# Performance work log

Hardware: AMD Instinct MI355X
Metric: run time of the kernel (lower is better)

## Reference

```python
import jax, jax.numpy as jnp
import numpy as np

B, S, D, H, DFF = 2, 2048, 1024, 16, 4096
DK = D // H
EPS = float(np.finfo(np.float32).eps)  # torch RMSNorm default eps = finfo eps


def rmsnorm(x, g):
    var = jnp.mean(x * x, axis=-1, keepdims=True)
    return x * jax.lax.rsqrt(var + EPS) * g


def rope_cos_sin(seq_len, dim, base=10000.0):
    inv_freq = 1.0 / (base ** (jnp.arange(0, dim, 2, dtype=jnp.float32) / dim))
    t = jnp.arange(seq_len, dtype=jnp.float32)
    freqs = jnp.outer(t, inv_freq)            # [S, dim/2]
    emb = jnp.concatenate([freqs, freqs], -1)  # [S, dim]
    return jnp.cos(emb), jnp.sin(emb)


def rotate_half(x):
    x1, x2 = x[..., : x.shape[-1] // 2], x[..., x.shape[-1] // 2:]
    return jnp.concatenate([-x2, x1], axis=-1)


def setup_inputs() -> dict:
    key = jax.random.key(0)
    ks = jax.random.split(key, 16)
    sc = 0.02
    return {
        "x": jax.random.normal(ks[0], (B, S, D), jnp.float32),
        "wq": jax.random.normal(ks[1], (D, D), jnp.float32) * sc,
        "bq": jnp.zeros((D,), jnp.float32),
        "wk": jax.random.normal(ks[2], (D, D), jnp.float32) * sc,
        "bk": jnp.zeros((D,), jnp.float32),
        "wv": jax.random.normal(ks[3], (D, D), jnp.float32) * sc,
        "bv": jnp.zeros((D,), jnp.float32),
        "wo": jax.random.normal(ks[4], (D, D), jnp.float32) * sc,
        "bo": jnp.zeros((D,), jnp.float32),
        "w1": jax.random.normal(ks[5], (D, DFF), jnp.float32) * sc,
        "b1": jnp.zeros((DFF,), jnp.float32),
        "w2": jax.random.normal(ks[6], (DFF, D), jnp.float32) * sc,
        "b2": jnp.zeros((D,), jnp.float32),
        "g1": jnp.ones((D,), jnp.float32),
        "g2": jnp.ones((D,), jnp.float32),
    }


def reference(x, wq, bq, wk, bk, wv, bv, wo, bo, w1, b1, w2, b2, g1, g2):
    b, s, d = x.shape
    # --- self-attention sublayer (pre-RMSNorm residual) ---
    h = rmsnorm(x, g1)
    q = (h @ wq + bq).reshape(b, s, H, DK).transpose(0, 2, 1, 3)  # [B,H,S,dk]
    k = (h @ wk + bk).reshape(b, s, H, DK).transpose(0, 2, 1, 3)
    v = (h @ wv + bv).reshape(b, s, H, DK).transpose(0, 2, 1, 3)
    cos, sin = rope_cos_sin(s, DK)
    cos = cos[None, None]  # [1,1,S,dk]
    sin = sin[None, None]
    q = q * cos + rotate_half(q) * sin
    k = k * cos + rotate_half(k) * sin
    scores = jnp.einsum("bhqd,bhkd->bhqk", q, k) / jnp.sqrt(jnp.float32(DK))
    p = jax.nn.softmax(scores, axis=-1)
    o = jnp.einsum("bhqk,bhkd->bhqd", p, v)
    o = o.transpose(0, 2, 1, 3).reshape(b, s, d)
    attn_out = o @ wo + bo
    x = x + attn_out
    # --- feed-forward sublayer ---
    h2 = rmsnorm(x, g2)
    ff = jax.nn.relu(h2 @ w1 + b1) @ w2 + b2
    return x + ff
```

## Files before the change

### kernel.cpp

```cpp
#include <hip/hip_runtime.h>
#include <math.h>

typedef unsigned short u16;
typedef __attribute__((ext_vector_type(8))) short bf16x8;
typedef __attribute__((ext_vector_type(4))) float f32x4;
typedef __attribute__((ext_vector_type(4))) unsigned int u32x4;

#define B_ 2
#define S_ 2048
#define D_ 1024
#define H_ 16
#define DK_ 64
#define DFF_ 4096
#define EPS_ 1.1920928955078125e-07f
#define EXP2SC 0.18033688011112042f

__device__ __forceinline__ float bf2f(u16 u) {
  unsigned int v = ((unsigned int)u) << 16;
  return __builtin_bit_cast(float, v);
}
__device__ __forceinline__ u16 f2bf(float f) {
  unsigned int x = __builtin_bit_cast(unsigned int, f);
  x += 0x7fffu + ((x >> 16) & 1u);
  return (u16)(x >> 16);
}

#if __has_builtin(__builtin_amdgcn_exp2f)
__device__ __forceinline__ float exp2r(float x) { return __builtin_amdgcn_exp2f(x); }
#else
__device__ __forceinline__ float exp2r(float x) { return exp2f(x); }
#endif

typedef __attribute__((address_space(3))) unsigned int lds_uint;
typedef const __attribute__((address_space(1))) unsigned int glb_uint;
__device__ __forceinline__ void gload16(const void* g, void* l) {
  __builtin_amdgcn_global_load_lds((glb_uint*)g, (lds_uint*)l, 16, 0, 0);
}

template <int N>
__device__ __forceinline__ void waitcnt_vm() {
  if constexpr (N == 8) asm volatile("s_waitcnt vmcnt(8)" ::: "memory");
  else if constexpr (N == 6) asm volatile("s_waitcnt vmcnt(6)" ::: "memory");
  else if constexpr (N == 4) asm volatile("s_waitcnt vmcnt(4)" ::: "memory");
  else if constexpr (N == 3) asm volatile("s_waitcnt vmcnt(3)" ::: "memory");
  else asm volatile("s_waitcnt vmcnt(0)" ::: "memory");
}

__device__ __forceinline__ unsigned int cvtpk(float lo, float hi) {
  unsigned int d;
  asm("v_cvt_pk_bf16_f32 %0, %1, %2" : "=v"(d) : "v"(lo), "v"(hi));
  return d;
}
__device__ __forceinline__ void plswap32(unsigned int& a, unsigned int& b) {
  asm("v_permlane32_swap_b32 %0, %1" : "+v"(a), "+v"(b));
}
__device__ __forceinline__ void plswap16(unsigned int& a, unsigned int& b) {
  asm("v_permlane16_swap_b32 %0, %1" : "+v"(a), "+v"(b));
}

__device__ __forceinline__ void xcd_swizzle(int& bx, int& by) {
  const int nx = gridDim.x;
  const int nwg = nx * gridDim.y;
  const int lin = blockIdx.y * nx + blockIdx.x;
  const int swz = (lin & 7) * (nwg >> 3) + (lin >> 3);
  bx = swz % nx;
  by = swz / nx;
}

__device__ __forceinline__ void xcd_swizzle3(int& bx, int& by, int& bz) {
  const int gx = gridDim.x, gy = gridDim.y, gz = gridDim.z;
  const int nb = gx * gy * gz;
  const int lin = ((int)blockIdx.z * gy + blockIdx.y) * gx + blockIdx.x;
  const int w = (lin & 7) * (nb >> 3) + (lin >> 3);
  bz = w % gz;
  const int r = w / gz;
  bx = r % gx;
  by = r / gx;
}

__global__ __launch_bounds__(256) void prep_qkvo(
    const float* __restrict__ wq, const float* __restrict__ wk,
    const float* __restrict__ wv, const float* __restrict__ wo,
    u16* __restrict__ qkvT, u16* __restrict__ woT,
    float* __restrict__ cosT, float* __restrict__ sinT) {
  __shared__ float t[32][33];
  const int bid = blockIdx.x;
  const int tid = threadIdx.x;
  if (bid < 4096) {
    const int m = bid >> 10;
    const int tb = bid & 1023;
    const float* src = (m == 0) ? wq : (m == 1) ? wk : (m == 2) ? wv : wo;
    u16* dst = (m == 3) ? woT : qkvT + (size_t)m * D_ * D_;
    const int c0 = (tb & 31) * 32, r0 = (tb >> 5) * 32;
    const int tx = tid & 31, ty = tid >> 5;
#pragma unroll
    for (int i = 0; i < 32; i += 8)
      t[ty + i][tx] = src[(size_t)(r0 + ty + i) * D_ + (c0 + tx)];
    __syncthreads();
#pragma unroll
    for (int i = 0; i < 32; i += 8)
      dst[(size_t)(c0 + ty + i) * D_ + (r0 + tx)] = f2bf(t[tx][ty + i]);
  } else {
    const int idx = (bid - 4096) * 256 + tid;
    const int s = idx >> 5, i = idx & 31;
    double inv = exp(((double)(-2 * i) / (double)DK_) * log(10000.0));
    double ang = (double)s * inv;
    cosT[idx] = (float)cos(ang);
    sinT[idx] = (float)sin(ang);
  }
}

__global__ __launch_bounds__(256) void prep_w12(
    const float* __restrict__ w1, const float* __restrict__ w2,
    u16* __restrict__ w1T, u16* __restrict__ w2T) {
  __shared__ float t[32][33];
  const int bid = blockIdx.x;
  const int tid = threadIdx.x;
  const int tx = tid & 31, ty = tid >> 5;
  if (bid < 4096) {
    const int c0 = (bid & 127) * 32, r0 = (bid >> 7) * 32;
#pragma unroll
    for (int i = 0; i < 32; i += 8)
      t[ty + i][tx] = w1[(size_t)(r0 + ty + i) * DFF_ + (c0 + tx)];
    __syncthreads();
#pragma unroll
    for (int i = 0; i < 32; i += 8)
      w1T[(size_t)(c0 + ty + i) * D_ + (r0 + tx)] = f2bf(t[tx][ty + i]);
  } else {
    const int b2 = bid - 4096;
    const int c0 = (b2 & 31) * 32, r0 = (b2 >> 5) * 32;
#pragma unroll
    for (int i = 0; i < 32; i += 8)
      t[ty + i][tx] = w2[(size_t)(r0 + ty + i) * D_ + (c0 + tx)];
    __syncthreads();
#pragma unroll
    for (int i = 0; i < 32; i += 8)
      w2T[(size_t)(c0 + ty + i) * DFF_ + (r0 + tx)] = f2bf(t[tx][ty + i]);
  }
}

__global__ __launch_bounds__(256) void rmsnorm_k(const float* __restrict__ X,
                                                 const float* __restrict__ g,
                                                 u16* __restrict__ out) {
  const int row = blockIdx.x;
  const float* xr = X + (size_t)row * D_;
  u16* orow = out + (size_t)row * D_;
  const int tid = threadIdx.x;
  float vals[4];
  float s = 0.f;
#pragma unroll
  for (int j = 0; j < 4; j++) {
    float v = xr[tid + j * 256];
    vals[j] = v;
    s += v * v;
  }
#pragma unroll
  for (int off = 32; off > 0; off >>= 1) s += __shfl_down(s, off, 64);
  __shared__ float red[4];
  __shared__ float ssc;
  int lane = tid & 63, wave = tid >> 6;
  if (lane == 0) red[wave] = s;
  __syncthreads();
  if (tid == 0) ssc = 1.0f / sqrtf((red[0] + red[1] + red[2] + red[3]) * (1.0f / D_) + EPS_);
  __syncthreads();
  float sc = ssc;
#pragma unroll
  for (int j = 0; j < 4; j++) {
    int i = tid + j * 256;
    orow[i] = f2bf(vals[j] * sc * g[i]);
  }
}

#define GK_STAGE(BU, K0)                                                               \
  _Pragma("unroll")                                                                    \
  for (int c = wave; c < BM / 16; c += 4) {                                            \
    const u16* gp = gkA + (size_t)(m0 + c * 16 + lrow) * gkLD + (K0) + lcol;           \
    gload16(gp, (char*)As + __builtin_amdgcn_readfirstlane((BU) * (BM * 64) + c * 1024)); \
  }                                                                                    \
  _Pragma("unroll")                                                                    \
  for (int c = wave; c < BN / 16; c += 4) {                                            \
    const u16* gp = gkB + (size_t)(n0 + c * 16 + lrow) * gkLD + (K0) + lcol;           \
    gload16(gp, (char*)Bs + __builtin_amdgcn_readfirstlane((BU) * (BN * 64) + c * 1024)); \
  }

#define GK_COMPUTE(BU)                                                                 \
  {                                                                                    \
    bf16x8 af[WR], bfv[WC];                                                            \
    _Pragma("unroll")                                                                  \
    for (int i = 0; i < WR; i++)                                                       \
      af[i] = *(const bf16x8*)&As[(BU) * (BM * 32) + (wm + i * 16 + l16) * 32 + quad * 8]; \
    _Pragma("unroll")                                                                  \
    for (int j = 0; j < WC; j++)                                                       \
      bfv[j] = *(const bf16x8*)&Bs[(BU) * (BN * 32) + (wn + j * 16 + l16) * 32 + quad * 8]; \
    _Pragma("unroll")                                                                  \
    for (int i = 0; i < WR; i++)                                                       \
      _Pragma("unroll")                                                                \
      for (int j = 0; j < WC; j++)                                                     \
        acc[i][j] = __builtin_amdgcn_mfma_f32_16x16x32_bf16(af[i], bfv[j], acc[i][j], 0, 0, 0); \
  }

#define GEMM_KLOOP(APTR, BPTR, KLEN, KLD)                                              \
  {                                                                                    \
    const u16* gkA = (APTR);                                                           \
    const u16* gkB = (BPTR);                                                           \
    const int gkLD = (KLD);                                                            \
    GK_STAGE(0, 0)                                                                     \
    GK_STAGE(1, 32)                                                                    \
    int gkcur = 0;                                                                     \
    for (int k0 = 0; k0 < (KLEN); k0 += 32) {                                          \
      if (k0 + 32 < (KLEN)) waitcnt_vm<WR / 2 + WC / 2>();       \
      else waitcnt_vm<0>();                                      \
      __builtin_amdgcn_s_barrier();                                                    \
      GK_COMPUTE(gkcur)                                                                \
      __builtin_amdgcn_s_barrier();                             \
      if (k0 + 64 < (KLEN)) { GK_STAGE(gkcur, k0 + 64) }                               \
      gkcur ^= 1;                                                                      \
    }                                                                                  \
  }

#define GK64_STAGE(BU, K0)                                                             \
  _Pragma("unroll")                                                                    \
  for (int p = 0; p < 2; p++) {                                                        \
    _Pragma("unroll")                                                                  \
    for (int c = wave; c < BM / 16; c += 4) {                                          \
      const u16* gp = gkA + (size_t)(m0 + c * 16 + lrow) * gkLD + (K0) + p * 32 + lcol; \
      gload16(gp, (char*)As + __builtin_amdgcn_readfirstlane((BU) * (BM * 128) + p * (BM * 64) + c * 1024)); \
    }                                                                                  \
    _Pragma("unroll")                                                                  \
    for (int c = wave; c < BN / 16; c += 4) {                                          \
      const u16* gp = gkB + (size_t)(n0 + c * 16 + lrow) * gkLD + (K0) + p * 32 + lcol; \
      gload16(gp, (char*)Bs + __builtin_amdgcn_readfirstlane((BU) * (BN * 128) + p * (BN * 64) + c * 1024)); \
    }                                                                                  \
  }

#define GK64_COMPUTE(BU)                                                               \
  _Pragma("unroll")                                                                    \
  for (int p = 0; p < 2; p++) {                                                        \
    bf16x8 af[WR], bfv[WC];                                                            \
    _Pragma("unroll")                                                                  \
    for (int i = 0; i < WR; i++)                                                       \
      af[i] = *(const bf16x8*)&As[(BU) * (BM * 64) + p * (BM * 32) + (wm + i * 16 + l16) * 32 + quad * 8]; \
    _Pragma("unroll")                                                                  \
    for (int j = 0; j < WC; j++)                                                       \
      bfv[j] = *(const bf16x8*)&Bs[(BU) * (BN * 64) + p * (BN * 32) + (wn + j * 16 + l16) * 32 + quad * 8]; \
    _Pragma("unroll")                                                                  \
    for (int i = 0; i < WR; i++)                                                       \
      _Pragma("unroll")                                                                \
      for (int j = 0; j < WC; j++)                                                     \
        acc[i][j] = __builtin_amdgcn_mfma_f32_16x16x32_bf16(af[i], bfv[j], acc[i][j], 0, 0, 0); \
  }

#define GEMM_KLOOP64(APTR, BPTR, KLEN, KLD)                                            \
  {                                                                                    \
    const u16* gkA = (APTR);                                                           \
    const u16* gkB = (BPTR);                                                           \
    const int gkLD = (KLD);                                                            \
    GK64_STAGE(0, 0)                                                                   \
    GK64_STAGE(1, 64)                                                                  \
    int gkcur = 0;                                                                     \
    for (int k0 = 0; k0 < (KLEN); k0 += 64) {                                          \
      if (k0 + 64 < (KLEN)) waitcnt_vm<WR + WC>();   \
      else waitcnt_vm<0>();                                      \
      __builtin_amdgcn_s_barrier();                                                    \
      GK64_COMPUTE(gkcur)                                                              \
      __builtin_amdgcn_s_barrier();                         \
      if (k0 + 128 < (KLEN)) { GK64_STAGE(gkcur, k0 + 128) }                           \
      gkcur ^= 1;                                                                      \
    }                                                                                  \
  }

template <int MODE, int WR, int WC>
__global__ __launch_bounds__(256, 4) void gemm_bt(
    const u16* __restrict__ A, const u16* __restrict__ Bt, const float* __restrict__ bias,
    u16* __restrict__ outB, float* __restrict__ outF, const float* __restrict__ resF,
    int M, int N, int K) {
  constexpr int BM = 2 * WR * 16;
  constexpr int BN = 2 * WC * 16;
  __shared__ u16 As[2 * BM * 32];
  __shared__ u16 Bs[2 * BN * 32];
  const int tid = threadIdx.x;
  const int wave = tid >> 6, lane = tid & 63, quad = lane >> 4, l16 = lane & 15;
  const int wm = (wave >> 1) * (WR * 16), wn = (wave & 1) * (WC * 16);
  int bx, by;
  xcd_swizzle(bx, by);
  const int m0 = by * BM, n0 = bx * BN;
  const int lrow = lane >> 2, lcol = (lane & 3) * 8;
  f32x4 acc[WR][WC] = {};
  GEMM_KLOOP(A, Bt, K, K)
#pragma unroll
  for (int i = 0; i < WR; i++)
#pragma unroll
    for (int j = 0; j < WC; j++) {
      int col = n0 + wn + j * 16 + l16;
      float bv = bias[col];
#pragma unroll
      for (int r = 0; r < 4; r++) {
        int row = m0 + wm + i * 16 + quad * 4 + r;
        size_t off = (size_t)row * N + col;
        float v = acc[i][j][r] + bv;
        if constexpr (MODE == 1) v = fmaxf(v, 0.f);
        if constexpr (MODE == 2) outF[off] = v + resF[off];
        else outB[off] = f2bf(v);
      }
    }
}

__global__ __launch_bounds__(256, 4) void gemm_qkv(
    const u16* __restrict__ A, const u16* __restrict__ Bt,
    const float* __restrict__ bq, const float* __restrict__ bk, const float* __restrict__ bv,
    const float* __restrict__ cosT, const float* __restrict__ sinT,
    u16* __restrict__ Qb, u16* __restrict__ Kb, u16* __restrict__ VT, int M, int K) {
  constexpr int WR = 4, WC = 4;
  constexpr int BM = 128, BN = 128;
  __shared__ u16 As[2 * BM * 32];
  __shared__ u16 Bs[2 * BN * 32];
  const int tid = threadIdx.x;
  const int wave = tid >> 6, lane = tid & 63, quad = lane >> 4, l16 = lane & 15;
  const int wm = (wave >> 1) * 64, wn = (wave & 1) * 64;
  int bx, by;
  xcd_swizzle(bx, by);
  const int m0 = by * BM, n0 = bx * BN;
  const int lrow = lane >> 2, lcol = (lane & 3) * 8;
  f32x4 acc[WR][WC] = {};
  GEMM_KLOOP(A, Bt, K, K)
  const int g = n0 >> 10;
  if (g < 2) {
    u16* dst = (g == 0) ? Qb : Kb;
    const float* bias = (g == 0) ? bq : bk;
    const float scq = (g == 0) ? EXP2SC : 1.0f;
#pragma unroll
    for (int i = 0; i < WR; i++)
#pragma unroll
      for (int jp = 0; jp < 2; jp++) {
        int col0 = n0 + wn + jp * 16 + l16;
        int c0 = col0 & 1023;
        float bv0 = bias[c0], bv1 = bias[c0 + 32];
        int irot = jp * 16 + l16;
        int row0 = m0 + wm + i * 16 + quad * 4;
#pragma unroll
        for (int r = 0; r < 4; r++) {
          int row = row0 + r;
          int s2 = row & 2047;
          float cs = cosT[s2 * 32 + irot];
          float sn = sinT[s2 * 32 + irot];
          float x0 = acc[i][jp][r] + bv0;
          float x1 = acc[i][jp + 2][r] + bv1;
          dst[(size_t)row * D_ + c0]      = f2bf((x0 * cs - x1 * sn) * scq);
          dst[(size_t)row * D_ + c0 + 32] = f2bf((x1 * cs + x0 * sn) * scq);
        }
      }
  } else {
#pragma unroll
    for (int i = 0; i < WR; i++)
#pragma unroll
      for (int j = 0; j < WC; j++) {
        int col = n0 + wn + j * 16 + l16;
        int c = col & 1023;
        float bvv = bv[c];
        int row0 = m0 + wm + i * 16 + quad * 4;
        int hh = c >> 6, dk = c & 63;
        int b = row0 >> 11, s2 = row0 & 2047;
        ushort4 pv;
        pv.x = f2bf(acc[i][j][0] + bvv);
        pv.y = f2bf(acc[i][j][1] + bvv);
        pv.z = f2bf(acc[i][j][2] + bvv);
        pv.w = f2bf(acc[i][j][3] + bvv);
        *(ushort4*)&VT[(((size_t)(b * H_ + hh)) * DK_ + dk) * S_ + s2] = pv;
      }
  }
}

template <int WR, int WC>
__global__ __launch_bounds__(256) void gemm_splitk(
    const u16* __restrict__ A, const u16* __restrict__ Bt, const float* __restrict__ bias,
    float* outF, int M, int N, int Kslice, int Kld) {
  constexpr int BM = 2 * WR * 16;
  constexpr int BN = 2 * WC * 16;
  __shared__ u16 As[2 * BM * 64];
  __shared__ u16 Bs[2 * BN * 64];
  const int tid = threadIdx.x;
  const int wave = tid >> 6, lane = tid & 63, quad = lane >> 4, l16 = lane & 15;
  const int wm = (wave >> 1) * (WR * 16), wn = (wave & 1) * (WC * 16);
  int bx, by, bz;
  xcd_swizzle3(bx, by, bz);
  const int m0 = by * BM, n0 = bx * BN;
  const int lrow = lane >> 2, lcol = (lane & 3) * 8;
  const u16* Ao = A + (size_t)bz * Kslice;
  const u16* Bo = Bt + (size_t)bz * Kslice;
  f32x4 acc[WR][WC] = {};
  GEMM_KLOOP64(Ao, Bo, Kslice, Kld)
  const bool addb = (bz == 0);
#pragma unroll
  for (int i = 0; i < WR; i++)
#pragma unroll
    for (int j = 0; j < WC; j++) {
      int col = n0 + wn + j * 16 + l16;
      float bv = addb ? bias[col] : 0.f;
#pragma unroll
      for (int r = 0; r < 4; r++) {
        int row = m0 + wm + i * 16 + quad * 4 + r;
        unsafeAtomicAdd(&outF[(size_t)row * N + col], acc[i][j][r] + bv);
      }
    }
}

__device__ __forceinline__ void softmax_pack(f32x4 s0, f32x4 s1, f32x4 s2, f32x4 s3,
                                             bf16x8& pf0, bf16x8& pf1) {
  f32x4 p0, p1, p2, p3;
#pragma unroll
  for (int r = 0; r < 4; r++) {
    p0[r] = exp2r(s0[r]);
    p1[r] = exp2r(s1[r]);
    p2[r] = exp2r(s2[r]);
    p3[r] = exp2r(s3[r]);
  }
  unsigned int X0 = cvtpk(p0[0], p0[1]), X1 = cvtpk(p0[2], p0[3]);
  unsigned int Y0 = cvtpk(p1[0], p1[1]), Y1 = cvtpk(p1[2], p1[3]);
  unsigned int Z0 = cvtpk(p2[0], p2[1]), Z1 = cvtpk(p2[2], p2[3]);
  unsigned int W0 = cvtpk(p3[0], p3[1]), W1 = cvtpk(p3[2], p3[3]);
  plswap32(X0, Y0); plswap16(X0, Y0);
  plswap32(X1, Y1); plswap16(X1, Y1);
  plswap32(Z0, W0); plswap16(Z0, W0);
  plswap32(Z1, W1); plswap16(Z1, W1);
  u32x4 lo = {X0, X1, Y0, Y1};
  u32x4 hi = {Z0, Z1, W0, W1};
  pf0 = __builtin_bit_cast(bf16x8, lo);
  pf1 = __builtin_bit_cast(bf16x8, hi);
}

__global__ __launch_bounds__(256, 4) void flash_attn(u16* __restrict__ Q,
                                                     const u16* __restrict__ Kg,
                                                     const u16* __restrict__ VT) {
  const int bh = blockIdx.y;
  const int b = bh >> 4, h = bh & 15;
  const int q0 = blockIdx.x * 128;
  const int tid = threadIdx.x;
  const int wave = tid >> 6, lane = tid & 63, quad = lane >> 4, l16 = lane & 15;
  const size_t base = (size_t)b * S_ * D_ + h * DK_;
  const size_t vbase = (size_t)bh * DK_ * S_;

  __shared__ u16 Ks[2][4096];
  __shared__ u16 Vts[2][4096];

  const int srow8 = lane >> 3;
  const int scol = ((lane & 7) ^ srow8) * 8;
  const int kkey = wave * 16 + srow8;
  const u16* kp0 = Kg + base + (size_t)kkey * D_ + scol;
  const int vdk = wave * 16 + srow8;
  const u16* vp0 = VT + vbase + (size_t)vdk * S_ + scol;

#define FA_STAGE(BU, KT)                                                               \
  _Pragma("unroll")                                                                    \
  for (int c = 0; c < 2; c++) {                                                        \
    gload16(kp0 + (size_t)((KT) + c * 8) * D_,                                         \
            (char*)Ks + __builtin_amdgcn_readfirstlane((BU) * 8192 + wave * 2048 + c * 1024)); \
    gload16(vp0 + (size_t)(c * 8) * S_ + (KT),                                         \
            (char*)Vts + __builtin_amdgcn_readfirstlane((BU) * 8192 + wave * 2048 + c * 1024)); \
  }

  FA_STAGE(0, 0)
  FA_STAGE(1, 64)

  const size_t qoffA = base + (size_t)(q0 + wave * 32 + l16) * D_ + quad * 8;
  const size_t qoffB = qoffA + (size_t)16 * D_;
  bf16x8 qa0 = *(const bf16x8*)(Q + qoffA);
  bf16x8 qa1 = *(const bf16x8*)(Q + qoffA + 32);
  bf16x8 qb0 = *(const bf16x8*)(Q + qoffB);
  bf16x8 qb1 = *(const bf16x8*)(Q + qoffB + 32);

  f32x4 oa[4] = {}, ob[4] = {};
  f32x4 lsa_acc = {}, lsb_acc = {};
  const u32x4 onesu = {0x3F803F80u, 0x3F803F80u, 0x3F803F80u, 0x3F803F80u};
  const bf16x8 ones = __builtin_bit_cast(bf16x8, onesu);
  const int sw = (l16 & 7) << 4;

#define FA_TILE(BU)                                                                    \
  {                                                                                    \
    const char* KsB = (const char*)Ks + (BU) * 8192;                                   \
    const char* VtsB = (const char*)Vts + (BU) * 8192;                                 \
    f32x4 sa[4] = {}, sb[4] = {};                                                      \
    __builtin_amdgcn_s_setprio(1);                                                     \
    _Pragma("unroll")                                                                  \
    for (int nt = 0; nt < 4; nt++) {                                                   \
      const char* krow = KsB + (nt * 16 + l16) * 128;                                  \
      bf16x8 k0 = *(const bf16x8*)(krow + ((quad * 16) ^ sw));                         \
      bf16x8 k1 = *(const bf16x8*)(krow + ((64 + quad * 16) ^ sw));                    \
      sa[nt] = __builtin_amdgcn_mfma_f32_16x16x32_bf16(k0, qa0, sa[nt], 0, 0, 0);      \
      sa[nt] = __builtin_amdgcn_mfma_f32_16x16x32_bf16(k1, qa1, sa[nt], 0, 0, 0);      \
      sb[nt] = __builtin_amdgcn_mfma_f32_16x16x32_bf16(k0, qb0, sb[nt], 0, 0, 0);      \
      sb[nt] = __builtin_amdgcn_mfma_f32_16x16x32_bf16(k1, qb1, sb[nt], 0, 0, 0);      \
    }                                                                                  \
    __builtin_amdgcn_s_setprio(0);                                                     \
    bf16x8 pa0, pa1, pb0, pb1;                                                         \
    softmax_pack(sa[0], sa[1], sa[2], sa[3], pa0, pa1);                                \
    softmax_pack(sb[0], sb[1], sb[2], sb[3], pb0, pb1);                                \
    __builtin_amdgcn_s_setprio(1);                                                     \
    lsa_acc = __builtin_amdgcn_mfma_f32_16x16x32_bf16(pa0, ones, lsa_acc, 0, 0, 0);    \
    lsa_acc = __builtin_amdgcn_mfma_f32_16x16x32_bf16(pa1, ones, lsa_acc, 0, 0, 0);    \
    lsb_acc = __builtin_amdgcn_mfma_f32_16x16x32_bf16(pb0, ones, lsb_acc, 0, 0, 0);    \
    lsb_acc = __builtin_amdgcn_mfma_f32_16x16x32_bf16(pb1, ones, lsb_acc, 0, 0, 0);    \
    _Pragma("unroll")                                                                  \
    for (int nt = 0; nt < 4; nt++) {                                                   \
      const char* vrow = VtsB + (nt * 16 + l16) * 128;                                 \
      bf16x8 v0 = *(const bf16x8*)(vrow + ((quad * 16) ^ sw));                         \
      bf16x8 v1 = *(const bf16x8*)(vrow + ((64 + quad * 16) ^ sw));                    \
      oa[nt] = __builtin_amdgcn_mfma_f32_16x16x32_bf16(pa0, v0, oa[nt], 0, 0, 0);      \
      oa[nt] = __builtin_amdgcn_mfma_f32_16x16x32_bf16(pa1, v1, oa[nt], 0, 0, 0);      \
      ob[nt] = __builtin_amdgcn_mfma_f32_16x16x32_bf16(pb0, v0, ob[nt], 0, 0, 0);      \
      ob[nt] = __builtin_amdgcn_mfma_f32_16x16x32_bf16(pb1, v1, ob[nt], 0, 0, 0);      \
    }                                                                                  \
    __builtin_amdgcn_s_setprio(0);                                                     \
  }

  int cur = 0;
  for (int kt = 0; kt < S_; kt += 64) {
    if (kt + 64 < S_) waitcnt_vm<4>();
    else waitcnt_vm<0>();
    __builtin_amdgcn_s_barrier();
    FA_TILE(cur)
    __builtin_amdgcn_s_barrier();
    if (kt + 128 < S_) { FA_STAGE(cur, kt + 128) }
    cur ^= 1;
  }
#undef FA_STAGE
#undef FA_TILE

#pragma unroll
  for (int r = 0; r < 4; r++) {
    float inva = 1.0f / lsa_acc[r];
    float invb = 1.0f / lsb_acc[r];
    const size_t aoff = base + (size_t)(q0 + wave * 32 + quad * 4 + r) * D_;
    const size_t boff = aoff + (size_t)16 * D_;
#pragma unroll
    for (int nt = 0; nt < 4; nt++) {
      Q[aoff + nt * 16 + l16] = f2bf(oa[nt][r] * inva);
      Q[boff + nt * 16 + l16] = f2bf(ob[nt][r] * invb);
    }
  }
}

extern "C" void kernel_launch(void* const* d_in, const int* in_sizes, int n_in,
                              void* d_out, int out_size, void* d_ws, size_t ws_size,
                              hipStream_t stream) {
  const float* x  = (const float*)d_in[0];
  const float* wq = (const float*)d_in[1];
  const float* bq = (const float*)d_in[2];
  const float* wk = (const float*)d_in[3];
  const float* bk = (const float*)d_in[4];
  const float* wv = (const float*)d_in[5];
  const float* bv = (const float*)d_in[6];
  const float* wo = (const float*)d_in[7];
  const float* bo = (const float*)d_in[8];
  const float* w1 = (const float*)d_in[9];
  const float* b1 = (const float*)d_in[10];
  const float* w2 = (const float*)d_in[11];
  const float* b2 = (const float*)d_in[12];
  const float* g1 = (const float*)d_in[13];
  const float* g2 = (const float*)d_in[14];

  char* ws = (char*)d_ws;
  const size_t MB = 1024 * 1024;
  u16* qkvT = (u16*)(ws + 0 * MB);
  u16* woT  = (u16*)(ws + 6 * MB);
  u16* h    = (u16*)(ws + 8 * MB);
  u16* Qb   = (u16*)(ws + 16 * MB);
  u16* Kb   = (u16*)(ws + 24 * MB);
  float* cosT = (float*)(ws + 32 * MB);
  float* sinT = (float*)(ws + 32 * MB + 256 * 1024);
  u16* w2T  = (u16*)(ws + 0 * MB);
  u16* w1T  = (u16*)(ws + 16 * MB);
  u16* f1   = (u16*)(ws + 24 * MB);
  u16* h2   = h;
  u16* Ob   = Qb;
  u16* VT   = (u16*)d_out;
  float* x2 = (float*)d_out;
  const bool bigffn = (ws_size >= 57 * MB);

  const int MS = B_ * S_;
  prep_qkvo<<<4096 + S_ * 32 / 256, 256, 0, stream>>>(wq, wk, wv, wo, qkvT, woT, cosT, sinT);
  rmsnorm_k<<<MS, 256, 0, stream>>>(x, g1, h);
  gemm_qkv<<<dim3(3 * D_ / 128, MS / 128), 256, 0, stream>>>(h, qkvT, bq, bk, bv, cosT, sinT, Qb, Kb, VT, MS, D_);
  flash_attn<<<dim3(S_ / 128, B_ * H_), 256, 0, stream>>>(Qb, Kb, VT);
  gemm_bt<2, 4, 2><<<dim3(D_ / 64, MS / 128), 256, 0, stream>>>(Ob, woT, bo, nullptr, x2, x, MS, D_, D_);

  prep_w12<<<8192, 256, 0, stream>>>(w1, w2, w1T, w2T);
  rmsnorm_k<<<MS, 256, 0, stream>>>(x2, g2, h2);
  if (bigffn) {
    gemm_bt<1, 4, 4><<<dim3(DFF_ / 128, MS / 128), 256, 0, stream>>>(h2, w1T, b1, f1, nullptr, nullptr, MS, DFF_, D_);
    gemm_splitk<4, 4><<<dim3(D_ / 128, MS / 128, 2), 256, 0, stream>>>(f1, w2T, b2, x2, MS, D_, 2048, DFF_);
  } else {
    for (int i = 0; i < 2; i++) {
      const u16* h2h = h2 + (size_t)i * 2048 * D_;
      float* x2h = x2 + (size_t)i * 2048 * D_;
      gemm_bt<1, 4, 4><<<dim3(DFF_ / 128, 2048 / 128), 256, 0, stream>>>(h2h, w1T, b1, f1, nullptr, nullptr, 2048, DFF_, D_);
      gemm_splitk<4, 4><<<dim3(D_ / 128, 2048 / 128, 4), 256, 0, stream>>>(f1, w2T, b2, x2h, 2048, D_, 1024, DFF_);
    }
  }
  (void)in_sizes; (void)n_in; (void)out_size;
}
```

Before: 340.1 us.

## Add 256x256-tile 512-thread GEMM for FFN up-projection

Adds a new GEMM kernel that computes 256x256 output tiles with 8 waves, using BK=64 double-buffered LDS staging and fused bias plus ReLU. It replaces the 128x128 gemm_bt for the w1 projection in both FFN paths. Larger tiles raise arithmetic intensity and cut global reloads of A and B. The cost is 128KB of LDS and a large accumulator register file, which allows only one block per CU. The grid also becomes small: 16x16 = 256 blocks on the big path and 128 blocks per half on the other path, which can hurt CU utilisation and tail balance.

Result: no change. 339.7 us (-0.1%).

```diff
diff --git a/kernel.cpp b/kernel.cpp
--- a/kernel.cpp
+++ b/kernel.cpp
@@ -301,6 +301,91 @@
         if constexpr (MODE == 1) v = fmaxf(v, 0.f);
         if constexpr (MODE == 2) outF[off] = v + resF[off];
         else outB[off] = f2bf(v);
+      }
+    }
+}
+
+__global__ __launch_bounds__(512, 1) void gemm_256(
+    const u16* __restrict__ A, const u16* __restrict__ Bt, const float* __restrict__ bias,
+    u16* __restrict__ outB, int M, int N, int K) {
+  __shared__ u16 As[32768];
+  __shared__ u16 Bs[32768];
+  const int tid = threadIdx.x;
+  const int wave = tid >> 6, lane = tid & 63, quad = lane >> 4, l16 = lane & 15;
+  const int wm2 = wave >> 2;
+  const int wn2 = wave & 3;
+  int bx, by;
+  xcd_swizzle(bx, by);
+  const int m0 = by * 256, n0 = bx * 256;
+  const int srow = lane >> 2, scol = (lane & 3) * 8;
+
+#define STG256(BU, KT)                                                                 \
+  _Pragma("unroll")                                                                    \
+  for (int hf = 0; hf < 2; hf++)                                                       \
+    _Pragma("unroll")                                                                  \
+    for (int p = 0; p < 2; p++) {                                                      \
+      gload16(A + (size_t)(m0 + hf * 128 + wave * 16 + srow) * K + (KT) + p * 32 + scol, \
+              (char*)As + __builtin_amdgcn_readfirstlane((BU) * 32768 + hf * 16384 + p * 8192 + wave * 1024)); \
+      gload16(Bt + (size_t)(n0 + hf * 128 + wave * 16 + srow) * K + (KT) + p * 32 + scol, \
+              (char*)Bs + __builtin_amdgcn_readfirstlane((BU) * 32768 + hf * 16384 + p * 8192 + wave * 1024)); \
+    }
+
+#define QUAD256(BU, RH, CH)                                                            \
+  {                                                                                    \
+    bf16x8 af[4][2], bfv[2][2];                                                        \
+    _Pragma("unroll")                                                                  \
+    for (int i = 0; i < 4; i++)                                                        \
+      _Pragma("unroll")                                                                \
+      for (int p = 0; p < 2; p++)                                                      \
+        af[i][p] = *(const bf16x8*)&As[(BU) * 16384 + wm2 * 8192 + p * 4096 +          \
+                                       ((RH) * 64 + i * 16 + l16) * 32 + quad * 8];    \
+    _Pragma("unroll")                                                                  \
+    for (int j = 0; j < 2; j++)                                                        \
+      _Pragma("unroll")                                                                \
+      for (int p = 0; p < 2; p++)                                                      \
+        bfv[j][p] = *(const bf16x8*)&Bs[(BU) * 16384 + (wn2 >> 1) * 8192 + p * 4096 +  \
+                                        ((wn2 & 1) * 64 + (CH) * 32 + j * 16 + l16) * 32 + quad * 8]; \
+    _Pragma("unroll")                                                                  \
+    for (int i = 0; i < 4; i++)                                                        \
+      _Pragma("unroll")                                                                \
+      for (int j = 0; j < 2; j++)                                                      \
+        _Pragma("unroll")                                                              \
+        for (int p = 0; p < 2; p++)                                                    \
+          acc[(RH) * 4 + i][(CH) * 2 + j] = __builtin_amdgcn_mfma_f32_16x16x32_bf16(   \
+              af[i][p], bfv[j][p], acc[(RH) * 4 + i][(CH) * 2 + j], 0, 0, 0);          \
+  }
+
+  f32x4 acc[8][4] = {};
+  STG256(0, 0)
+  STG256(1, 64)
+  int cur = 0;
+  for (int k0 = 0; k0 < K; k0 += 64) {
+    if (k0 + 64 < K) waitcnt_vm<8>();
+    else waitcnt_vm<0>();
+    __builtin_amdgcn_s_barrier();
+    __builtin_amdgcn_s_setprio(1);
+    QUAD256(cur, 0, 0)
+    QUAD256(cur, 1, 0)
+    QUAD256(cur, 0, 1)
+    QUAD256(cur, 1, 1)
+    __builtin_amdgcn_s_setprio(0);
+    __builtin_amdgcn_s_barrier();
+    if (k0 + 128 < K) { STG256(cur, k0 + 128) }
+    cur ^= 1;
+  }
+#undef STG256
+#undef QUAD256
+
+#pragma unroll
+  for (int ri = 0; ri < 8; ri++)
+#pragma unroll
+    for (int ci = 0; ci < 4; ci++) {
+      int col = n0 + wn2 * 64 + (ci >> 1) * 32 + (ci & 1) * 16 + l16;
+      float bv = bias[col];
+#pragma unroll
+      for (int r = 0; r < 4; r++) {
+        int row = m0 + wm2 * 128 + (ri >> 2) * 64 + (ri & 3) * 16 + quad * 4 + r;
+        outB[(size_t)row * N + col] = f2bf(fmaxf(acc[ri][ci][r] + bv, 0.f));
       }
     }
 }
@@ -586,13 +671,13 @@
   prep_w12<<<8192, 256, 0, stream>>>(w1, w2, w1T, w2T);
   rmsnorm_k<<<MS, 256, 0, stream>>>(x2, g2, h2);
   if (bigffn) {
-    gemm_bt<1, 4, 4><<<dim3(DFF_ / 128, MS / 128), 256, 0, stream>>>(h2, w1T, b1, f1, nullptr, nullptr, MS, DFF_, D_);
+    gemm_256<<<dim3(DFF_ / 256, MS / 256), 512, 0, stream>>>(h2, w1T, b1, f1, MS, DFF_, D_);
     gemm_splitk<4, 4><<<dim3(D_ / 128, MS / 128, 2), 256, 0, stream>>>(f1, w2T, b2, x2, MS, D_, 2048, DFF_);
   } else {
     for (int i = 0; i < 2; i++) {
       const u16* h2h = h2 + (size_t)i * 2048 * D_;
       float* x2h = x2 + (size_t)i * 2048 * D_;
-      gemm_bt<1, 4, 4><<<dim3(DFF_ / 128, 2048 / 128), 256, 0, stream>>>(h2h, w1T, b1, f1, nullptr, nullptr, 2048, DFF_, D_);
+      gemm_256<<<dim3(DFF_ / 256, 2048 / 256), 512, 0, stream>>>(h2h, w1T, b1, f1, 2048, DFF_, D_);
       gemm_splitk<4, 4><<<dim3(D_ / 128, 2048 / 128, 4), 256, 0, stream>>>(f1, w2T, b2, x2h, 2048, D_, 1024, DFF_);
     }
   }
```
